# Performance work log

Measured on AMD Instinct MI355X. Metric: run time of the kernel, lower is better.

The kernel has to match this reference:

```python
import jax, jax.numpy as jnp
import numpy as np

B, S, D, H = 2, 2048, 1024, 16
HD = D // H

def setup_inputs() -> dict:
    key = jax.random.key(0)
    k1, k2, k3 = jax.random.split(key, 3)
    x = jax.random.normal(k1, (B, S, D), dtype=jnp.float32)
    c_attn_w = jax.random.normal(k2, (D, 3 * D), dtype=jnp.float32) * 0.02
    c_attn_b = jnp.zeros((3 * D,), dtype=jnp.float32)
    c_proj_w = jax.random.normal(k3, (D, D), dtype=jnp.float32) * 0.02
    c_proj_b = jnp.zeros((D,), dtype=jnp.float32)
    return {"x": x, "c_attn_w": c_attn_w, "c_attn_b": c_attn_b,
            "c_proj_w": c_proj_w, "c_proj_b": c_proj_b}

def reference(x, c_attn_w, c_attn_b, c_proj_w, c_proj_b):
    bsz, seq_len, d = x.shape
    # Conv1D: addmm(bias, x, weight) -> x @ W + b
    qkv = x @ c_attn_w + c_attn_b                      # [B,S,3D]
    xq, xk, xv = jnp.split(qkv, 3, axis=-1)
    # [B,H,S,hd]
    xq = xq.reshape(bsz, seq_len, H, HD).transpose(0, 2, 1, 3)
    xk = xk.reshape(bsz, seq_len, H, HD).transpose(0, 2, 1, 3)
    xv = xv.reshape(bsz, seq_len, H, HD).transpose(0, 2, 1, 3)
    # Eager attention: QK^T / sqrt(hd), causal mask, softmax, AV
    scale = jnp.asarray(HD, x.dtype) ** 0.5
    attn_weights = jnp.einsum('bhqd,bhkd->bhqk', xq, xk) / scale
    causal = jnp.tril(jnp.ones((seq_len, seq_len), dtype=bool))
    mask_value = jnp.finfo(attn_weights.dtype).min
    attn_weights = jnp.where(causal[None, None], attn_weights, mask_value)
    attn_weights = jax.nn.softmax(attn_weights, axis=-1)
    attn_output = jnp.einsum('bhqk,bhkd->bhqd', attn_weights, xv)  # [B,H,S,hd]
    attn_output = attn_output.transpose(0, 2, 1, 3).reshape(bsz, seq_len, d)
    attn_output = attn_output @ c_proj_w + c_proj_b
    return attn_output
```

## Files before the change

kernel.cpp:

```cpp
#include <hip/hip_runtime.h>
#include <hip/hip_bf16.h>
#include <stdint.h>

#define S_LEN 2048
#define D_DIM 1024
#define N_HEAD 16

typedef unsigned short u16;
typedef __attribute__((ext_vector_type(4))) float f32x4;
typedef __attribute__((ext_vector_type(16))) float f32x16;
typedef __attribute__((ext_vector_type(8))) short bf16x8;
typedef __attribute__((ext_vector_type(4))) unsigned short u16x4;
typedef __attribute__((ext_vector_type(4))) float flt4;

#define MFMA16(a, b, c) __builtin_amdgcn_mfma_f32_16x16x32_bf16((a), (b), (c), 0, 0, 0)
#define MFMA32(a, b, c) __builtin_amdgcn_mfma_f32_32x32x16_bf16((a), (b), (c), 0, 0, 0)

__device__ __forceinline__ u16 f32_bf16(float f) {
    union { float f; uint32_t u; } x;
    x.f = f;
    uint32_t r = (x.u + 0x7FFFu + ((x.u >> 16) & 1u)) >> 16;
    return (u16)r;
}

__device__ __forceinline__ uint32_t pack2(float a, float b) {
    __hip_bfloat162 h = __float22bfloat162_rn(float2{a, b});
    return *(uint32_t*)&h;
}

__device__ __forceinline__ void gload_lds16(const void* g, void* l) {
    __builtin_amdgcn_global_load_lds(
        (const __attribute__((address_space(1))) unsigned int*)(uintptr_t)g,
        (__attribute__((address_space(3))) unsigned int*)(uint32_t)(uintptr_t)l,
        16, 0, 0);
}


__global__ __launch_bounds__(256) void cvt_bf16_kernel(const float* __restrict__ in,
                                                       u16* __restrict__ out, int n) {
    int i = (blockIdx.x * 256 + threadIdx.x) * 4;
    if (i < n) {
        flt4 v = *(const flt4*)(in + i);
        u16x4 u;
        u[0] = f32_bf16(v[0]); u[1] = f32_bf16(v[1]);
        u[2] = f32_bf16(v[2]); u[3] = f32_bf16(v[3]);
        *(u16x4*)(out + i) = u;
    }
}

__global__ __launch_bounds__(256) void transpose_cvt_kernel(const float* __restrict__ in,
                                                            u16* __restrict__ out,
                                                            int R, int C) {
    __shared__ float tile[32][33];
    int tc = blockIdx.x * 32, tr = blockIdx.y * 32;
    int lx = threadIdx.x & 31, ly = threadIdx.x >> 5;
#pragma unroll
    for (int i = 0; i < 32; i += 8)
        tile[ly + i][lx] = in[(size_t)(tr + ly + i) * C + tc + lx];
    __syncthreads();
#pragma unroll
    for (int i = 0; i < 32; i += 8)
        out[(size_t)(tc + ly + i) * R + tr + lx] = f32_bf16(tile[lx][ly + i]);
}


template <int MODE>
__global__ __launch_bounds__(256)
void gemm_bt_kernel(const u16* __restrict__ A, const u16* __restrict__ Bt,
                    const float* __restrict__ bias,
                    float* __restrict__ outF,
                    u16* __restrict__ qo, u16* __restrict__ ko, u16* __restrict__ vto,
                    int M, int N, int K) {
    __shared__ u16 As[128 * 32];
    __shared__ u16 Bs[128 * 32];
    const int tid = threadIdx.x;
    const int w = tid >> 6, lane = tid & 63;
    const int lr = lane & 15, lg = lane >> 4;
    const int bm = blockIdx.y * 128, bn = blockIdx.x * 128;
    const int wr = w >> 1, wc = w & 1;

    f32x4 acc[4][4];
#pragma unroll
    for (int m = 0; m < 4; m++)
#pragma unroll
        for (int n = 0; n < 4; n++) acc[m][n] = (f32x4){0.f, 0.f, 0.f, 0.f};

    const u16* Abase = A + (size_t)(bm + (tid >> 2)) * K + (tid & 3) * 8;
    const u16* Bbase = Bt + (size_t)(bn + (tid >> 2)) * K + (tid & 3) * 8;
    u16* AsW = As + w * 512;
    u16* BsW = Bs + w * 512;

    for (int kt = 0; kt < K; kt += 32) {
        gload_lds16(Abase + kt, AsW);
        gload_lds16(Abase + kt + (size_t)64 * K, AsW + 2048);
        gload_lds16(Bbase + kt, BsW);
        gload_lds16(Bbase + kt + (size_t)64 * K, BsW + 2048);
        __syncthreads();

        bf16x8 a[4], b[4];
        const bf16x8* Av = (const bf16x8*)As;
        const bf16x8* Bv = (const bf16x8*)Bs;
#pragma unroll
        for (int m = 0; m < 4; m++) a[m] = Av[(wr * 64 + m * 16 + lr) * 4 + lg];
#pragma unroll
        for (int n = 0; n < 4; n++) b[n] = Bv[(wc * 64 + n * 16 + lr) * 4 + lg];
#pragma unroll
        for (int m = 0; m < 4; m++)
#pragma unroll
            for (int n = 0; n < 4; n++)
                acc[m][n] = MFMA16(a[m], b[n], acc[m][n]);
        __syncthreads();
    }

    const int rowb = bm + wr * 64, colb = bn + wc * 64;
    if (MODE == 0) {
#pragma unroll
        for (int m = 0; m < 4; m++)
#pragma unroll
            for (int j = 0; j < 4; j++) {
                int r = rowb + m * 16 + lg * 4 + j;
                size_t base = (size_t)r * N;
#pragma unroll
                for (int n = 0; n < 4; n++) {
                    int c = colb + n * 16 + lr;
                    outF[base + c] = acc[m][n][j] + bias[c];
                }
            }
    } else {
#pragma unroll
        for (int m = 0; m < 4; m++)
#pragma unroll
            for (int j = 0; j < 4; j++) {
                int r = rowb + m * 16 + lg * 4 + j;
                int bb = r >> 11, s = r & (S_LEN - 1);
#pragma unroll
                for (int n = 0; n < 4; n++) {
                    int c = colb + n * 16 + lr;
                    float v = acc[m][n][j] + bias[c];
                    int part = c >> 10, cc = c & (D_DIM - 1);
                    if (part == 0) v *= 0.125f * 1.44269504f;
                    u16 bv = f32_bf16(v);
                    int h = cc >> 6, d = cc & 63;
                    size_t bh = (size_t)(bb * N_HEAD + h);
                    if (part == 0)      qo[(bh * S_LEN + s) * 64 + d] = bv;
                    else if (part == 1) ko[(bh * S_LEN + s) * 64 + d] = bv;
                    else                vto[(bh * 64 + d) * S_LEN + s] = bv;
                }
            }
    }
}


__global__ __launch_bounds__(128, 2)
void flash_attn_kernel(const u16* __restrict__ Qg, const u16* __restrict__ Kg,
                       const u16* __restrict__ Vt, u16* __restrict__ Og) {
    const int id = blockIdx.x;
    const int bh = id & 31;
    const int p  = id >> 5;
    const int w = threadIdx.x >> 6;
    const int lane = threadIdx.x & 63;
    const int ql = lane & 31, hi = lane >> 5;
    const int qbA = p * 32, qbB = (63 - p) * 32;
    const int last = 63 - p;

    const u16* Qh = Qg + (size_t)bh * S_LEN * 64;
    const u16* Kh = Kg + (size_t)bh * S_LEN * 64;
    const u16* Vh = Vt + (size_t)bh * 64 * S_LEN;

    __shared__ float mbuf[2][64][34];

    bf16x8 qfA[4], qfB[4];
#pragma unroll
    for (int c = 0; c < 4; c++) {
        qfA[c] = *(const bf16x8*)(Qh + (size_t)(qbA + ql) * 64 + c * 16 + hi * 8);
        qfB[c] = *(const bf16x8*)(Qh + (size_t)(qbB + ql) * 64 + c * 16 + hi * 8);
    }

    f32x16 otA0 = {}, otA1 = {}, otB0 = {}, otB1 = {};
    float mA = -1e30f, lA = 0.f, mB = -1e30f, lB = 0.f;

    auto loadKV = [&](int t, bf16x8 (&k)[4], bf16x8 (&v)[4]) {
        const u16* kp = Kh + ((size_t)t * 32 + ql) * 64 + hi * 8;
#pragma unroll
        for (int c = 0; c < 4; c++) k[c] = *(const bf16x8*)(kp + c * 16);
        const size_t kv0 = (size_t)t * 32;
#pragma unroll
        for (int u = 0; u < 4; u++)
            v[u] = *(const bf16x8*)(Vh + ((size_t)((u >> 1) * 32 + ql)) * S_LEN + kv0 + (u & 1) * 16 + hi * 8);
    };

    auto softpv = [&](const f32x16& st, bool diag, float& m, float& l,
                      f32x16& o0, f32x16& o1, const bf16x8 (&v)[4]) {
        float s[16];
#pragma unroll
        for (int r = 0; r < 16; r++) s[r] = st[r];
        if (diag) {
#pragma unroll
            for (int r = 0; r < 16; r++) {
                int kvl = ((r & 3) + 8 * (r >> 2)) + 4 * hi;
                if (kvl > ql) s[r] = -1e30f;
            }
        }
        float t0 = fmaxf(s[0], s[1]),   t1 = fmaxf(s[2], s[3]);
        float t2 = fmaxf(s[4], s[5]),   t3 = fmaxf(s[6], s[7]);
        float t4 = fmaxf(s[8], s[9]),   t5 = fmaxf(s[10], s[11]);
        float t6 = fmaxf(s[12], s[13]), t7 = fmaxf(s[14], s[15]);
        t0 = fmaxf(t0, t1); t2 = fmaxf(t2, t3); t4 = fmaxf(t4, t5); t6 = fmaxf(t6, t7);
        float tmax = fmaxf(fmaxf(t0, t2), fmaxf(t4, t6));
        tmax = fmaxf(tmax, __shfl_xor(tmax, 32));

        float corr = 1.f;
        if (!__all(tmax <= m)) {
            float mn = fmaxf(m, tmax);
            corr = __builtin_amdgcn_exp2f(m - mn);
            m = mn;
            o0 *= corr;
            o1 *= corr;
        }
        float pe[16];
        float rs = 0.f;
#pragma unroll
        for (int r = 0; r < 16; r++) { pe[r] = __builtin_amdgcn_exp2f(s[r] - m); rs += pe[r]; }
        rs += __shfl_xor(rs, 32);
        l = l * corr + rs;

        uint32_t wv[8];
#pragma unroll
        for (int sp = 0; sp < 8; sp++) wv[sp] = pack2(pe[2 * sp], pe[2 * sp + 1]);
        auto r02 = __builtin_amdgcn_permlane32_swap(wv[0], wv[2], false, false);
        auto r13 = __builtin_amdgcn_permlane32_swap(wv[1], wv[3], false, false);
        auto r46 = __builtin_amdgcn_permlane32_swap(wv[4], wv[6], false, false);
        auto r57 = __builtin_amdgcn_permlane32_swap(wv[5], wv[7], false, false);
        union { uint32_t u[4]; bf16x8 v; } pa0, pa1;
        pa0.u[0] = r02[0]; pa0.u[1] = r13[0]; pa0.u[2] = r02[1]; pa0.u[3] = r13[1];
        pa1.u[0] = r46[0]; pa1.u[1] = r57[0]; pa1.u[2] = r46[1]; pa1.u[3] = r57[1];

        __builtin_amdgcn_s_setprio(1);
        o0 = MFMA32(v[0], pa0.v, o0);
        o0 = MFMA32(v[1], pa1.v, o0);
        o1 = MFMA32(v[2], pa0.v, o1);
        o1 = MFMA32(v[3], pa1.v, o1);
        __builtin_amdgcn_s_setprio(0);
    };

    auto step = [&](int t, const bf16x8 (&k)[4], const bf16x8 (&v)[4]) {
        const bool actA = (t <= p);
        f32x16 stA = {}, stB = {};
        __builtin_amdgcn_s_setprio(1);
        if (actA) {
#pragma unroll
            for (int c = 0; c < 4; c++) stA = MFMA32(k[c], qfA[c], stA);
        }
#pragma unroll
        for (int c = 0; c < 4; c++) stB = MFMA32(k[c], qfB[c], stB);
        __builtin_amdgcn_s_setprio(0);
        if (actA) softpv(stA, t == p, mA, lA, otA0, otA1, v);
        softpv(stB, t == last, mB, lB, otB0, otB1, v);
    };

    bf16x8 k0[4], v0[4], k1[4], v1[4];
    loadKV(w, k0, v0);
    int t = w;
    for (;;) {
        if (t + 2 <= last) loadKV(t + 2, k1, v1);
        step(t, k0, v0);
        t += 2;
        if (t > last) break;
        if (t + 2 <= last) loadKV(t + 2, k0, v0);
        step(t, k1, v1);
        t += 2;
        if (t > last) break;
    }

    if (w == 1) {
        float* bA = mbuf[0][lane];
        float* bB = mbuf[1][lane];
        bA[0] = mA; bA[1] = lA;
        bB[0] = mB; bB[1] = lB;
#pragma unroll
        for (int r = 0; r < 16; r++) {
            bA[2 + r] = otA0[r]; bA[18 + r] = otA1[r];
            bB[2 + r] = otB0[r]; bB[18 + r] = otB1[r];
        }
    }
    __syncthreads();
    if (w == 0) {
        const int bb = bh >> 4, hh = bh & 15;
        auto fin = [&](float m0, float l0, const f32x16& o0, const f32x16& o1,
                       const float* b, int qbase) {
            float m1 = b[0], l1 = b[1];
            float ms = fmaxf(m0, m1);
            float a0 = __builtin_amdgcn_exp2f(m0 - ms);
            float a1 = __builtin_amdgcn_exp2f(m1 - ms);
            float inv = 1.f / (l0 * a0 + l1 * a1);
            u16* orow = Og + ((size_t)(bb * S_LEN) + qbase + ql) * D_DIM + hh * 64;
#pragma unroll
            for (int rp = 0; rp < 8; rp++) {
                int r = rp * 2;
                int d = ((r & 3) + 8 * (r >> 2)) + 4 * hi;
                float x0 = (o0[r] * a0 + b[2 + r] * a1) * inv;
                float x1 = (o0[r + 1] * a0 + b[2 + r + 1] * a1) * inv;
                *(uint32_t*)(orow + d) = pack2(x0, x1);
                float y0 = (o1[r] * a0 + b[18 + r] * a1) * inv;
                float y1 = (o1[r + 1] * a0 + b[18 + r + 1] * a1) * inv;
                *(uint32_t*)(orow + 32 + d) = pack2(y0, y1);
            }
        };
        fin(mA, lA, otA0, otA1, mbuf[0][lane], qbA);
        fin(mB, lB, otB0, otB1, mbuf[1][lane], qbB);
    }
}


extern "C" void kernel_launch(void* const* d_in, const int* in_sizes, int n_in,
                              void* d_out, int out_size, void* d_ws, size_t ws_size,
                              hipStream_t stream) {
    const float* x  = (const float*)d_in[0];
    const float* w1 = (const float*)d_in[1];
    const float* b1 = (const float*)d_in[2];
    const float* w2 = (const float*)d_in[3];
    const float* b2 = (const float*)d_in[4];
    float* out = (float*)d_out;

    u16* ws  = (u16*)d_ws;
    u16* xb  = ws;
    u16* w1t = xb  + 4096 * 1024;
    u16* w2t = w1t + 3072 * 1024;
    u16* q   = w2t + 1024 * 1024;
    u16* k   = q   + 4194304;
    u16* vt  = k   + 4194304;
    u16* x2  = vt  + 4194304;

    cvt_bf16_kernel<<<dim3(4096), dim3(256), 0, stream>>>(x, xb, 4096 * 1024);
    transpose_cvt_kernel<<<dim3(3072 / 32, 1024 / 32), dim3(256), 0, stream>>>(w1, w1t, 1024, 3072);
    transpose_cvt_kernel<<<dim3(1024 / 32, 1024 / 32), dim3(256), 0, stream>>>(w2, w2t, 1024, 1024);

    gemm_bt_kernel<1><<<dim3(3072 / 128, 4096 / 128), dim3(256), 0, stream>>>(
        xb, w1t, b1, nullptr, q, k, vt, 4096, 3072, 1024);

    flash_attn_kernel<<<dim3(1024), dim3(128), 0, stream>>>(q, k, vt, x2);

    gemm_bt_kernel<0><<<dim3(1024 / 128, 4096 / 128), dim3(256), 0, stream>>>(
        x2, w2t, b2, out, nullptr, nullptr, nullptr, 4096, 1024, 1024);
}
```

Baseline: 218.5 us.

## Split attention KV loop across four waves and swizzle GEMM block order

The flash attention block grows from two to four waves. Each wave takes every fourth KV tile, and the four partial results are merged through LDS, with the partial outputs stored as bf16. The GEMM remaps block indices so that consecutive workgroups land in different groups, which aims at better cache locality across the chiplet dies. The softmax rescale is also skipped unless the new max exceeds the old one by a threshold, to cut rescale work. Risks are precision loss from the bf16 partials and from lazy rescaling, higher LDS and register pressure, and more merge work at the end.

```diff
diff --git a/kernel.cpp b/kernel.cpp
--- a/kernel.cpp
+++ b/kernel.cpp
@@ -26,6 +26,13 @@
 __device__ __forceinline__ uint32_t pack2(float a, float b) {
     __hip_bfloat162 h = __float22bfloat162_rn(float2{a, b});
     return *(uint32_t*)&h;
+}
+
+__device__ __forceinline__ float blo(uint32_t u) {
+    union { uint32_t u; float f; } x; x.u = u << 16; return x.f;
+}
+__device__ __forceinline__ float bhi(uint32_t u) {
+    union { uint32_t u; float f; } x; x.u = u & 0xFFFF0000u; return x.f;
 }
 
 __device__ __forceinline__ void gload_lds16(const void* g, void* l) {
@@ -76,7 +83,11 @@
     const int tid = threadIdx.x;
     const int w = tid >> 6, lane = tid & 63;
     const int lr = lane & 15, lg = lane >> 4;
-    const int bm = blockIdx.y * 128, bn = blockIdx.x * 128;
+    const int gx = gridDim.x;
+    const int nwg = gx * gridDim.y;
+    const int wg = blockIdx.y * gx + blockIdx.x;
+    const int swz = (wg & 7) * (nwg >> 3) + (wg >> 3);
+    const int bm = (swz / gx) * 128, bn = (swz % gx) * 128;
     const int wr = w >> 1, wc = w & 1;
 
     f32x4 acc[4][4];
@@ -151,7 +162,7 @@
 }
 
 
-__global__ __launch_bounds__(128, 2)
+__global__ __launch_bounds__(256, 4)
 void flash_attn_kernel(const u16* __restrict__ Qg, const u16* __restrict__ Kg,
                        const u16* __restrict__ Vt, u16* __restrict__ Og) {
     const int id = blockIdx.x;
@@ -167,7 +178,8 @@
     const u16* Kh = Kg + (size_t)bh * S_LEN * 64;
     const u16* Vh = Vt + (size_t)bh * 64 * S_LEN;
 
-    __shared__ float mbuf[2][64][34];
+    __shared__ __align__(4) u16 obuf[2][3][64][34];
+    __shared__ float mlbuf[2][3][64][3];
 
     bf16x8 qfA[4], qfB[4];
 #pragma unroll
@@ -180,13 +192,13 @@
     float mA = -1e30f, lA = 0.f, mB = -1e30f, lB = 0.f;
 
     auto loadKV = [&](int t, bf16x8 (&k)[4], bf16x8 (&v)[4]) {
-        const u16* kp = Kh + ((size_t)t * 32 + ql) * 64 + hi * 8;
+        const u16* kp = Kh + (size_t)t * 2048 + ql * 64 + hi * 8;
 #pragma unroll
         for (int c = 0; c < 4; c++) k[c] = *(const bf16x8*)(kp + c * 16);
-        const size_t kv0 = (size_t)t * 32;
+        const u16* vp = Vh + (size_t)ql * S_LEN + t * 32 + hi * 8;
 #pragma unroll
         for (int u = 0; u < 4; u++)
-            v[u] = *(const bf16x8*)(Vh + ((size_t)((u >> 1) * 32 + ql)) * S_LEN + kv0 + (u & 1) * 16 + hi * 8);
+            v[u] = *(const bf16x8*)(vp + (size_t)((u >> 1) * 32) * S_LEN + (u & 1) * 16);
     };
 
     auto softpv = [&](const f32x16& st, bool diag, float& m, float& l,
@@ -201,16 +213,16 @@
                 if (kvl > ql) s[r] = -1e30f;
             }
         }
-        float t0 = fmaxf(s[0], s[1]),   t1 = fmaxf(s[2], s[3]);
-        float t2 = fmaxf(s[4], s[5]),   t3 = fmaxf(s[6], s[7]);
-        float t4 = fmaxf(s[8], s[9]),   t5 = fmaxf(s[10], s[11]);
-        float t6 = fmaxf(s[12], s[13]), t7 = fmaxf(s[14], s[15]);
-        t0 = fmaxf(t0, t1); t2 = fmaxf(t2, t3); t4 = fmaxf(t4, t5); t6 = fmaxf(t6, t7);
-        float tmax = fmaxf(fmaxf(t0, t2), fmaxf(t4, t6));
+        float u0 = fmaxf(fmaxf(s[0], s[1]), s[2]);
+        float u1 = fmaxf(fmaxf(s[3], s[4]), s[5]);
+        float u2 = fmaxf(fmaxf(s[6], s[7]), s[8]);
+        float u3 = fmaxf(fmaxf(s[9], s[10]), s[11]);
+        float u4 = fmaxf(fmaxf(s[12], s[13]), s[14]);
+        float tmax = fmaxf(fmaxf(fmaxf(u0, u1), u2), fmaxf(fmaxf(u3, u4), s[15]));
         tmax = fmaxf(tmax, __shfl_xor(tmax, 32));
 
         float corr = 1.f;
-        if (!__all(tmax <= m)) {
+        if (!__all(tmax <= m + 11.5f)) {
             float mn = fmaxf(m, tmax);
             corr = __builtin_amdgcn_exp2f(m - mn);
             m = mn;
@@ -262,52 +274,69 @@
     loadKV(w, k0, v0);
     int t = w;
     for (;;) {
-        if (t + 2 <= last) loadKV(t + 2, k1, v1);
+        if (t + 4 <= last) loadKV(t + 4, k1, v1);
         step(t, k0, v0);
-        t += 2;
+        t += 4;
         if (t > last) break;
-        if (t + 2 <= last) loadKV(t + 2, k0, v0);
+        if (t + 4 <= last) loadKV(t + 4, k0, v0);
         step(t, k1, v1);
-        t += 2;
+        t += 4;
         if (t > last) break;
     }
 
-    if (w == 1) {
-        float* bA = mbuf[0][lane];
-        float* bB = mbuf[1][lane];
-        bA[0] = mA; bA[1] = lA;
-        bB[0] = mB; bB[1] = lB;
-#pragma unroll
-        for (int r = 0; r < 16; r++) {
-            bA[2 + r] = otA0[r]; bA[18 + r] = otA1[r];
-            bB[2 + r] = otB0[r]; bB[18 + r] = otB1[r];
+    if (w > 0) {
+        const int wi = w - 1;
+        u16* oA = obuf[0][wi][lane];
+        u16* oB = obuf[1][wi][lane];
+#pragma unroll
+        for (int rp = 0; rp < 8; rp++) {
+            int r = rp * 2;
+            *(uint32_t*)(oA + r)      = pack2(otA0[r], otA0[r + 1]);
+            *(uint32_t*)(oA + 16 + r) = pack2(otA1[r], otA1[r + 1]);
+            *(uint32_t*)(oB + r)      = pack2(otB0[r], otB0[r + 1]);
+            *(uint32_t*)(oB + 16 + r) = pack2(otB1[r], otB1[r + 1]);
         }
+        mlbuf[0][wi][lane][0] = mA; mlbuf[0][wi][lane][1] = lA;
+        mlbuf[1][wi][lane][0] = mB; mlbuf[1][wi][lane][1] = lB;
     }
     __syncthreads();
     if (w == 0) {
         const int bb = bh >> 4, hh = bh & 15;
         auto fin = [&](float m0, float l0, const f32x16& o0, const f32x16& o1,
-                       const float* b, int qbase) {
-            float m1 = b[0], l1 = b[1];
-            float ms = fmaxf(m0, m1);
+                       int qi, int qbase) {
+            float mw0 = mlbuf[qi][0][lane][0], lw0 = mlbuf[qi][0][lane][1];
+            float mw1 = mlbuf[qi][1][lane][0], lw1 = mlbuf[qi][1][lane][1];
+            float mw2 = mlbuf[qi][2][lane][0], lw2 = mlbuf[qi][2][lane][1];
+            float ms = fmaxf(fmaxf(m0, mw0), fmaxf(mw1, mw2));
             float a0 = __builtin_amdgcn_exp2f(m0 - ms);
-            float a1 = __builtin_amdgcn_exp2f(m1 - ms);
-            float inv = 1.f / (l0 * a0 + l1 * a1);
+            float a1 = __builtin_amdgcn_exp2f(mw0 - ms);
+            float a2 = __builtin_amdgcn_exp2f(mw1 - ms);
+            float a3 = __builtin_amdgcn_exp2f(mw2 - ms);
+            float inv = 1.f / (l0 * a0 + lw0 * a1 + lw1 * a2 + lw2 * a3);
+            const u16* r0 = obuf[qi][0][lane];
+            const u16* r1 = obuf[qi][1][lane];
+            const u16* r2 = obuf[qi][2][lane];
             u16* orow = Og + ((size_t)(bb * S_LEN) + qbase + ql) * D_DIM + hh * 64;
 #pragma unroll
             for (int rp = 0; rp < 8; rp++) {
                 int r = rp * 2;
                 int d = ((r & 3) + 8 * (r >> 2)) + 4 * hi;
-                float x0 = (o0[r] * a0 + b[2 + r] * a1) * inv;
-                float x1 = (o0[r + 1] * a0 + b[2 + r + 1] * a1) * inv;
-                *(uint32_t*)(orow + d) = pack2(x0, x1);
-                float y0 = (o1[r] * a0 + b[18 + r] * a1) * inv;
-                float y1 = (o1[r + 1] * a0 + b[18 + r + 1] * a1) * inv;
-                *(uint32_t*)(orow + 32 + d) = pack2(y0, y1);
+                uint32_t ua = *(const uint32_t*)(r0 + r);
+                uint32_t ub = *(const uint32_t*)(r1 + r);
+                uint32_t uc = *(const uint32_t*)(r2 + r);
+                float x0 = o0[r] * a0 + blo(ua) * a1 + blo(ub) * a2 + blo(uc) * a3;
+                float x1 = o0[r + 1] * a0 + bhi(ua) * a1 + bhi(ub) * a2 + bhi(uc) * a3;
+                *(uint32_t*)(orow + d) = pack2(x0 * inv, x1 * inv);
+                ua = *(const uint32_t*)(r0 + 16 + r);
+                ub = *(const uint32_t*)(r1 + 16 + r);
+                uc = *(const uint32_t*)(r2 + 16 + r);
+                float y0 = o1[r] * a0 + blo(ua) * a1 + blo(ub) * a2 + blo(uc) * a3;
+                float y1 = o1[r + 1] * a0 + bhi(ua) * a1 + bhi(ub) * a2 + bhi(uc) * a3;
+                *(uint32_t*)(orow + 32 + d) = pack2(y0 * inv, y1 * inv);
             }
         };
-        fin(mA, lA, otA0, otA1, mbuf[0][lane], qbA);
-        fin(mB, lB, otB0, otB1, mbuf[1][lane], qbB);
+        fin(mA, lA, otA0, otA1, 0, qbA);
+        fin(mB, lB, otB0, otB1, 1, qbB);
     }
 }
 
@@ -338,7 +367,7 @@
     gemm_bt_kernel<1><<<dim3(3072 / 128, 4096 / 128), dim3(256), 0, stream>>>(
         xb, w1t, b1, nullptr, q, k, vt, 4096, 3072, 1024);
 
-    flash_attn_kernel<<<dim3(1024), dim3(128), 0, stream>>>(q, k, vt, x2);
+    flash_attn_kernel<<<dim3(1024), dim3(256), 0, stream>>>(q, k, vt, x2);
 
     gemm_bt_kernel<0><<<dim3(1024 / 128, 4096 / 128), dim3(256), 0, stream>>>(
         x2, w2t, b2, out, nullptr, nullptr, nullptr, 4096, 1024, 1024);
```

New measurement: 431.0 us. +97.2%, slower.

## Write V row-major from QKV GEMM, transpose via LDS kernel, swizzle tiles

Applied to the files above, without the earlier changes.

The QKV GEMM epilogue now writes Q, K and V all in a head-major row layout with per-block part selection. This replaces the scattered strided stores of transposed V with a separate LDS-tiled transpose kernel that uses vectorized accesses. The GEMM also remaps workgroup IDs with an XCD-style swizzle for cache locality. Flash attention switches to a 3-way max tree and defers rescaling until the running max grows by more than a threshold, which trades an extra kernel launch for cheaper stores and fewer rescales.

```diff
diff --git a/kernel.cpp b/kernel.cpp
--- a/kernel.cpp
+++ b/kernel.cpp
@@ -11,6 +11,7 @@
 typedef __attribute__((ext_vector_type(16))) float f32x16;
 typedef __attribute__((ext_vector_type(8))) short bf16x8;
 typedef __attribute__((ext_vector_type(4))) unsigned short u16x4;
+typedef __attribute__((ext_vector_type(8))) unsigned short u16x8;
 typedef __attribute__((ext_vector_type(4))) float flt4;
 
 #define MFMA16(a, b, c) __builtin_amdgcn_mfma_f32_16x16x32_bf16((a), (b), (c), 0, 0, 0)
@@ -63,20 +64,48 @@
         out[(size_t)(tc + ly + i) * R + tr + lx] = f32_bf16(tile[lx][ly + i]);
 }
 
+__global__ __launch_bounds__(256) void v_transpose_kernel(const u16* __restrict__ Vin,
+                                                          u16* __restrict__ Vt) {
+    __shared__ u16 tile[64][72];
+    const int bh = blockIdx.y, st = blockIdx.x;
+    const int t = threadIdx.x;
+    const u16* src = Vin + ((size_t)bh * S_LEN + st * 64) * 64;
+    const int r = t >> 3, c = (t & 7) * 8;
+#pragma unroll
+    for (int i = 0; i < 2; i++) {
+        int rr = r + i * 32;
+        *(u16x8*)&tile[rr][c] = *(const u16x8*)(src + rr * 64 + c);
+    }
+    __syncthreads();
+    const int d = t & 63, sc = t >> 6;
+    u16x8 o0, o1;
+#pragma unroll
+    for (int j = 0; j < 8; j++) o0[j] = tile[sc * 16 + j][d];
+#pragma unroll
+    for (int j = 0; j < 8; j++) o1[j] = tile[sc * 16 + 8 + j][d];
+    u16* dst = Vt + ((size_t)bh * 64 + d) * S_LEN + st * 64 + sc * 16;
+    *(u16x8*)dst = o0;
+    *(u16x8*)(dst + 8) = o1;
+}
+
 
 template <int MODE>
 __global__ __launch_bounds__(256)
 void gemm_bt_kernel(const u16* __restrict__ A, const u16* __restrict__ Bt,
                     const float* __restrict__ bias,
                     float* __restrict__ outF,
-                    u16* __restrict__ qo, u16* __restrict__ ko, u16* __restrict__ vto,
+                    u16* __restrict__ qo, u16* __restrict__ ko, u16* __restrict__ vo,
                     int M, int N, int K) {
     __shared__ u16 As[128 * 32];
     __shared__ u16 Bs[128 * 32];
     const int tid = threadIdx.x;
     const int w = tid >> 6, lane = tid & 63;
     const int lr = lane & 15, lg = lane >> 4;
-    const int bm = blockIdx.y * 128, bn = blockIdx.x * 128;
+    const int gx = gridDim.x;
+    const int nwg = gx * gridDim.y;
+    const int wg = blockIdx.y * gx + blockIdx.x;
+    const int swz = (wg & 7) * (nwg >> 3) + (wg >> 3);
+    const int bm = (swz / gx) * 128, bn = (swz % gx) * 128;
     const int wr = w >> 1, wc = w & 1;
 
     f32x4 acc[4][4];
@@ -127,6 +156,10 @@
                 }
             }
     } else {
+        const int part = colb >> 10;
+        const int ccb = colb & (D_DIM - 1);
+        u16* dst = (part == 0) ? qo : (part == 1) ? ko : vo;
+        const float scale = (part == 0) ? 0.125f * 1.44269504f : 1.f;
 #pragma unroll
         for (int m = 0; m < 4; m++)
 #pragma unroll
@@ -136,15 +169,10 @@
 #pragma unroll
                 for (int n = 0; n < 4; n++) {
                     int c = colb + n * 16 + lr;
-                    float v = acc[m][n][j] + bias[c];
-                    int part = c >> 10, cc = c & (D_DIM - 1);
-                    if (part == 0) v *= 0.125f * 1.44269504f;
-                    u16 bv = f32_bf16(v);
+                    int cc = ccb + n * 16 + lr;
                     int h = cc >> 6, d = cc & 63;
-                    size_t bh = (size_t)(bb * N_HEAD + h);
-                    if (part == 0)      qo[(bh * S_LEN + s) * 64 + d] = bv;
-                    else if (part == 1) ko[(bh * S_LEN + s) * 64 + d] = bv;
-                    else                vto[(bh * 64 + d) * S_LEN + s] = bv;
+                    float v = (acc[m][n][j] + bias[c]) * scale;
+                    dst[((size_t)(bb * N_HEAD + h) * S_LEN + s) * 64 + d] = f32_bf16(v);
                 }
             }
     }
@@ -201,16 +229,16 @@
                 if (kvl > ql) s[r] = -1e30f;
             }
         }
-        float t0 = fmaxf(s[0], s[1]),   t1 = fmaxf(s[2], s[3]);
-        float t2 = fmaxf(s[4], s[5]),   t3 = fmaxf(s[6], s[7]);
-        float t4 = fmaxf(s[8], s[9]),   t5 = fmaxf(s[10], s[11]);
-        float t6 = fmaxf(s[12], s[13]), t7 = fmaxf(s[14], s[15]);
-        t0 = fmaxf(t0, t1); t2 = fmaxf(t2, t3); t4 = fmaxf(t4, t5); t6 = fmaxf(t6, t7);
-        float tmax = fmaxf(fmaxf(t0, t2), fmaxf(t4, t6));
+        float u0 = fmaxf(fmaxf(s[0], s[1]), s[2]);
+        float u1 = fmaxf(fmaxf(s[3], s[4]), s[5]);
+        float u2 = fmaxf(fmaxf(s[6], s[7]), s[8]);
+        float u3 = fmaxf(fmaxf(s[9], s[10]), s[11]);
+        float u4 = fmaxf(fmaxf(s[12], s[13]), s[14]);
+        float tmax = fmaxf(fmaxf(fmaxf(u0, u1), u2), fmaxf(fmaxf(u3, u4), s[15]));
         tmax = fmaxf(tmax, __shfl_xor(tmax, 32));
 
         float corr = 1.f;
-        if (!__all(tmax <= m)) {
+        if (!__all(tmax <= m + 11.5f)) {
             float mn = fmaxf(m, tmax);
             corr = __builtin_amdgcn_exp2f(m - mn);
             m = mn;
@@ -330,13 +358,16 @@
     u16* k   = q   + 4194304;
     u16* vt  = k   + 4194304;
     u16* x2  = vt  + 4194304;
+    u16* v   = x2;
 
     cvt_bf16_kernel<<<dim3(4096), dim3(256), 0, stream>>>(x, xb, 4096 * 1024);
     transpose_cvt_kernel<<<dim3(3072 / 32, 1024 / 32), dim3(256), 0, stream>>>(w1, w1t, 1024, 3072);
     transpose_cvt_kernel<<<dim3(1024 / 32, 1024 / 32), dim3(256), 0, stream>>>(w2, w2t, 1024, 1024);
 
     gemm_bt_kernel<1><<<dim3(3072 / 128, 4096 / 128), dim3(256), 0, stream>>>(
-        xb, w1t, b1, nullptr, q, k, vt, 4096, 3072, 1024);
+        xb, w1t, b1, nullptr, q, k, v, 4096, 3072, 1024);
+
+    v_transpose_kernel<<<dim3(S_LEN / 64, 32), dim3(256), 0, stream>>>(v, vt);
 
     flash_attn_kernel<<<dim3(1024), dim3(128), 0, stream>>>(q, k, vt, x2);
 
```

After: 232.9 us. +6.5%, slower.
